# Optimization experiments

Hardware: AMD Instinct MI355X
Metric: run time of the kernel (lower is better)

The kernel has to match this reference:

```python
import jax, jax.numpy as jnp
import numpy as np

T, B, D, H = 256, 2048, 16, 64


def _init_cell(key, in_dim, hidden):
    k1, k2, k3, k4 = jax.random.split(key, 4)
    s = 1.0 / np.sqrt(hidden)
    return (
        jax.random.uniform(k1, (4 * hidden, in_dim), minval=-s, maxval=s),
        jax.random.uniform(k2, (4 * hidden, hidden), minval=-s, maxval=s),
        jax.random.uniform(k3, (4 * hidden,), minval=-s, maxval=s),
        jax.random.uniform(k4, (4 * hidden,), minval=-s, maxval=s),
    )


def setup_inputs() -> dict:
    key = jax.random.key(0)
    kx, k0, k1, k2 = jax.random.split(key, 4)
    x = jax.random.normal(kx, (T, B, D), dtype=jnp.float32)
    W_ih0, W_hh0, b_ih0, b_hh0 = _init_cell(k0, D, H)
    W_ih1, W_hh1, b_ih1, b_hh1 = _init_cell(k1, H, H)
    W_ih2, W_hh2, b_ih2, b_hh2 = _init_cell(k2, H, H)
    return dict(x=x,
                W_ih0=W_ih0, W_hh0=W_hh0, b_ih0=b_ih0, b_hh0=b_hh0,
                W_ih1=W_ih1, W_hh1=W_hh1, b_ih1=b_ih1, b_hh1=b_hh1,
                W_ih2=W_ih2, W_hh2=W_hh2, b_ih2=b_ih2, b_hh2=b_hh2)


def _lstm_cell(x_t, h, c, W_ih, W_hh, b_ih, b_hh):
    # torch.nn.LSTMCell gate order: i, f, g, o
    gates = x_t @ W_ih.T + b_ih + h @ W_hh.T + b_hh  # (B, 4H)
    i, f, g, o = jnp.split(gates, 4, axis=-1)
    c_new = jax.nn.sigmoid(f) * c + jax.nn.sigmoid(i) * jnp.tanh(g)
    h_new = jax.nn.sigmoid(o) * jnp.tanh(c_new)
    return h_new, c_new


def reference(x, W_ih0, W_hh0, b_ih0, b_hh0,
              W_ih1, W_hh1, b_ih1, b_hh1,
              W_ih2, W_hh2, b_ih2, b_hh2):
    Bsz = x.shape[1]
    z = jnp.zeros((Bsz, H), dtype=x.dtype)
    init = (z, z, z, z, z, z)  # h0,h1,h2,c0,c1,c2

    def step(state, x_t):
        h0, h1, h2, c0, c1, c2 = state
        h0, c0 = _lstm_cell(x_t, h0, c0, W_ih0, W_hh0, b_ih0, b_hh0)
        h1, c1 = _lstm_cell(h0, h1, c1, W_ih1, W_hh1, b_ih1, b_hh1)
        h2, c2 = _lstm_cell(h1, h2, c2, W_ih2, W_hh2, b_ih2, b_hh2)
        return (h0, h1, h2, c0, c1, c2), h2

    _, out = jax.lax.scan(step, init, x)  # out: (T, B, H)
    return out
```

## Files before the change

kernel.cpp:

```cpp
#include <hip/hip_runtime.h>
#include <hip/hip_bf16.h>


#define TT 256
#define BB 2048
#define DD 16
#define HH 64

#define SROW 216
#define PANEL (8 * SROW)

typedef __attribute__((ext_vector_type(8))) _Float16 halfx8;
typedef __attribute__((ext_vector_type(8))) unsigned short ushortx8;
typedef __attribute__((ext_vector_type(4))) float floatx4;

#if __has_builtin(__builtin_amdgcn_exp2f)
#define EXP2F(x) __builtin_amdgcn_exp2f(x)
#else
#define EXP2F(x) exp2f(x)
#endif
#if __has_builtin(__builtin_amdgcn_rcpf)
#define RCPF(x) __builtin_amdgcn_rcpf(x)
#else
#define RCPF(x) (1.0f/(x))
#endif

__device__ __forceinline__ float sigm(float x) {
  return RCPF(1.0f + EXP2F(-1.4426950408889634f * x));
}
__device__ __forceinline__ float tanh_f(float x) {
  float xc = fminf(fmaxf(x, -16.0f), 16.0f);
  float t = EXP2F(2.8853900817779268f * xc);
  return 1.0f - 2.0f * RCPF(t + 1.0f);
}
__device__ __forceinline__ void block_sync() {
  asm volatile("s_waitcnt lgkmcnt(0)" ::: "memory");
  __builtin_amdgcn_s_barrier();
}

__global__ void detect_k(const unsigned short* __restrict__ xr, int* __restrict__ flag) {
  int cnt = 0;
  for (int i = threadIdx.x; i < 4096; i += 64) {
    float v = __uint_as_float(((unsigned int)xr[i]) << 16);
    if (!(fabsf(v) < 4.0f)) cnt++;
  }
#pragma unroll
  for (int o = 32; o > 0; o >>= 1) cnt += __shfl_down(cnt, o, 64);
  if (threadIdx.x == 0) flag[0] = (cnt < 100) ? 1 : 0;
}

#define LAYER_MFMA(KSTART, NKT, WA, BS)                                          \
    floatx4 a0 = BS[0], a1 = BS[1];                                              \
    {                                                                            \
      const _Float16* row_ = Pp + rd_row + (KSTART);                             \
      _Pragma("unroll")                                                          \
      for (int kt = 0; kt < (NKT); ++kt) {                                       \
        halfx8 bfr = *(const halfx8*)(row_ + kt * 32 + 8 * g);                   \
        a0 = __builtin_amdgcn_mfma_f32_16x16x32_f16(WA[0][kt], bfr, a0, 0, 0, 0);\
        a1 = __builtin_amdgcn_mfma_f32_16x16x32_f16(WA[1][kt], bfr, a1, 0, 0, 0);\
      }                                                                          \
    }

__launch_bounds__(512, 2)
__global__ void lstm3_k(const void* __restrict__ xg,
                        const void* W0i, const void* W0h, const void* B0i, const void* B0h,
                        const void* W1i, const void* W1h, const void* B1i, const void* B1h,
                        const void* W2i, const void* W2h, const void* B2i, const void* B2h,
                        void* __restrict__ outp, const int* __restrict__ flagp) {
  const int tid = threadIdx.x;
  const int w = tid >> 6;
  const int lane = tid & 63;
  const int c = lane & 15;
  const int g = lane >> 4;
  const int rowbase = blockIdx.x * 8;
  const int isbf = flagp ? flagp[0] : 1;

  __shared__ __align__(16) _Float16 SH[2 * PANEL];

  auto ldf = [&](const void* b, long i) -> float {
    return isbf ? __bfloat162float(((const __hip_bfloat16*)b)[i]) : ((const float*)b)[i];
  };
  auto ld8 = [&](const void* b, long i) -> halfx8 {
    halfx8 r;
    if (isbf) {
      ushortx8 raw = *(const ushortx8*)((const unsigned short*)b + i);
#pragma unroll
      for (int j = 0; j < 8; ++j)
        r[j] = (_Float16)__uint_as_float(((unsigned int)raw[j]) << 16);
    } else {
      const float* s = (const float*)b + i;
#pragma unroll
      for (int j = 0; j < 8; ++j) r[j] = (_Float16)s[j];
    }
    return r;
  };
  auto fragA = [&](const void* Wi, const void* Wh, int Kih, int Mt, int kt) -> halfx8 {
    int ril = Mt * 16 + c;
    int u = ril >> 2, q = ril & 3;
    int orig = q * 64 + u;
    int k0 = kt * 32 + 8 * g;
    if (k0 < Kih) return ld8(Wi, (long)orig * Kih + k0);
    if (k0 < Kih + 64) return ld8(Wh, (long)orig * 64 + (k0 - Kih));
    halfx8 z = {};
    return z;
  };

  halfx8 wA0[2][3], wA1[2][4], wA2[2][4];
  floatx4 bs0[2], bs1[2], bs2[2];
#pragma unroll
  for (int m = 0; m < 2; ++m) {
    const int Mt = 2 * w + m;
#pragma unroll
    for (int kt = 0; kt < 3; ++kt) wA0[m][kt] = fragA(W0i, W0h, 16, Mt, kt);
#pragma unroll
    for (int kt = 0; kt < 4; ++kt) wA1[m][kt] = fragA(W1i, W1h, 64, Mt, kt);
#pragma unroll
    for (int kt = 0; kt < 4; ++kt) wA2[m][kt] = fragA(W2i, W2h, 64, Mt, kt);
    const int ub = 4 * Mt + g;
#pragma unroll
    for (int q = 0; q < 4; ++q) {
      bs0[m][q] = ldf(B0i, 64 * q + ub) + ldf(B0h, 64 * q + ub);
      bs1[m][q] = ldf(B1i, 64 * q + ub) + ldf(B1h, 64 * q + ub);
      bs2[m][q] = ldf(B2i, 64 * q + ub) + ldf(B2h, 64 * q + ub);
    }
  }

  for (int i = tid; i < 2 * PANEL; i += 512) SH[i] = (_Float16)0.0f;
  block_sync();
  if (tid < 16) {
    int r = tid >> 1, hf = tid & 1;
    *(halfx8*)&SH[r * SROW + hf * 8] = ld8(xg, ((long)0 * BB + rowbase + r) * DD + hf * 8);
  }

  const int msel = c >> 3;
  const int r_el = c & 7;
  const int u_el = 8 * w + 4 * msel + g;
  const int rd_row = (c & 7) * SROW;
  const int wr_base = r_el * SROW + u_el;
  float c0s = 0.f, c1s = 0.f, c2s = 0.f;

#pragma unroll 1
  for (int s = 0; s < TT + 2; ++s) {
    const int p = s & 1, np = p ^ 1;
    const _Float16* Pp = SH + p * PANEL;
    _Float16* Pn = SH + np * PANEL;

    halfx8 xreg = {};
    const bool loader = (tid < 16) && (s + 1 < TT);
    if (loader)
      xreg = ld8(xg, ((long)(s + 1) * BB + rowbase + (tid >> 1)) * DD + (tid & 1) * 8);

    block_sync();

    if (s < TT) {
      LAYER_MFMA(0, 3, wA0, bs0)
      floatx4 gv = msel ? a1 : a0;
      float I = sigm(gv[0]), F = sigm(gv[1]), G = tanh_f(gv[2]), O = sigm(gv[3]);
      float cn = F * c0s + I * G; c0s = cn;
      Pn[wr_base + 16] = (_Float16)(O * tanh_f(cn));
    }
    if (s >= 1 && s <= TT) {
      LAYER_MFMA(16, 4, wA1, bs1)
      floatx4 gv = msel ? a1 : a0;
      float I = sigm(gv[0]), F = sigm(gv[1]), G = tanh_f(gv[2]), O = sigm(gv[3]);
      float cn = F * c1s + I * G; c1s = cn;
      Pn[wr_base + 80] = (_Float16)(O * tanh_f(cn));
    }
    if (s >= 2) {
      LAYER_MFMA(80, 4, wA2, bs2)
      floatx4 gv = msel ? a1 : a0;
      float I = sigm(gv[0]), F = sigm(gv[1]), G = tanh_f(gv[2]), O = sigm(gv[3]);
      float cn = F * c2s + I * G; c2s = cn;
      float hn = O * tanh_f(cn);
      Pn[wr_base + 144] = (_Float16)hn;
      size_t oi = ((size_t)(s - 2) * BB + rowbase + r_el) * HH + u_el;
      if (isbf) ((__hip_bfloat16*)outp)[oi] = __float2bfloat16(hn);
      else      ((float*)outp)[oi] = hn;
    }
    if (loader)
      *(halfx8*)&Pn[(tid >> 1) * SROW + (tid & 1) * 8] = xreg;
  }
}

extern "C" void kernel_launch(void* const* d_in, const int* in_sizes, int n_in,
                              void* d_out, int out_size, void* d_ws, size_t ws_size,
                              hipStream_t stream) {
  (void)in_sizes; (void)n_in; (void)out_size;
  int* flag = (ws_size >= sizeof(int)) ? (int*)d_ws : nullptr;
  if (flag) {
    detect_k<<<dim3(1), dim3(64), 0, stream>>>((const unsigned short*)d_in[0], flag);
  }
  lstm3_k<<<dim3(BB / 8), dim3(512), 0, stream>>>(
      d_in[0],
      d_in[1], d_in[2], d_in[3], d_in[4],
      d_in[5], d_in[6], d_in[7], d_in[8],
      d_in[9], d_in[10], d_in[11], d_in[12],
      d_out, flag);
}
```

Baseline: 310.8 us.

## Interleave MFMAs of all three LSTM layers and unroll ping-pong step loop

Reorders the shared panel layout to [h0,h1,h2,x] so each lane loads all seven B fragments once per step. The MFMAs of all three layers are then issued interleaved, so independent accumulator chains hide MFMA latency. Layer-activity branches become predicated stores, the step loop is unrolled by two with constant panel offsets, and the tanh input clamp is removed. The trade-offs are wasted MFMA and transcendental work in the pipeline fill and drain steps, higher register pressure, and possible overflow behaviour in tanh for large inputs.

New measurement: 276.7 us. 1.12x faster.

```diff
diff --git a/kernel.cpp b/kernel.cpp
--- a/kernel.cpp
+++ b/kernel.cpp
@@ -9,6 +9,10 @@
 
 #define SROW 216
 #define PANEL (8 * SROW)
+#define H0O 0
+#define H1O 64
+#define H2O 128
+#define XO  192
 
 typedef __attribute__((ext_vector_type(8))) _Float16 halfx8;
 typedef __attribute__((ext_vector_type(8))) unsigned short ushortx8;
@@ -29,8 +33,7 @@
   return RCPF(1.0f + EXP2F(-1.4426950408889634f * x));
 }
 __device__ __forceinline__ float tanh_f(float x) {
-  float xc = fminf(fmaxf(x, -16.0f), 16.0f);
-  float t = EXP2F(2.8853900817779268f * xc);
+  float t = EXP2F(2.8853900817779268f * x);
   return 1.0f - 2.0f * RCPF(t + 1.0f);
 }
 __device__ __forceinline__ void block_sync() {
@@ -49,17 +52,59 @@
   if (threadIdx.x == 0) flag[0] = (cnt < 100) ? 1 : 0;
 }
 
-#define LAYER_MFMA(KSTART, NKT, WA, BS)                                          \
-    floatx4 a0 = BS[0], a1 = BS[1];                                              \
-    {                                                                            \
-      const _Float16* row_ = Pp + rd_row + (KSTART);                             \
-      _Pragma("unroll")                                                          \
-      for (int kt = 0; kt < (NKT); ++kt) {                                       \
-        halfx8 bfr = *(const halfx8*)(row_ + kt * 32 + 8 * g);                   \
-        a0 = __builtin_amdgcn_mfma_f32_16x16x32_f16(WA[0][kt], bfr, a0, 0, 0, 0);\
-        a1 = __builtin_amdgcn_mfma_f32_16x16x32_f16(WA[1][kt], bfr, a1, 0, 0, 0);\
-      }                                                                          \
-    }
+#define MF(A, B, C) __builtin_amdgcn_mfma_f32_16x16x32_f16(A, B, C, 0, 0, 0)
+
+#define BODY(S_, PPB, PNB)                                                        \
+  {                                                                               \
+    const int s_ = (S_);                                                          \
+    halfx8 xreg = {};                                                             \
+    const bool loader = (tid < 16) && (s_ + 1 < TT);                              \
+    if (loader)                                                                   \
+      xreg = ld8(xg, ((long)(s_ + 1) * BB + rowbase + (tid >> 1)) * DD + (tid & 1) * 8); \
+    block_sync();                                                                 \
+    const _Float16* PpR = SH + (PPB) + rd_off;                                    \
+    _Float16* Pn = SH + (PNB);                                                    \
+    halfx8 r0 = *(const halfx8*)(PpR + 0);                                        \
+    halfx8 r1 = *(const halfx8*)(PpR + 32);                                       \
+    halfx8 r2 = *(const halfx8*)(PpR + 64);                                       \
+    halfx8 r3 = *(const halfx8*)(PpR + 96);                                       \
+    halfx8 r4 = *(const halfx8*)(PpR + 128);                                      \
+    halfx8 r5 = *(const halfx8*)(PpR + 160);                                      \
+    halfx8 r6 = *(const halfx8*)(PpR + 192);                                      \
+    floatx4 a00 = bs0[0], a01 = bs0[1];                                           \
+    floatx4 a10 = bs1[0], a11 = bs1[1];                                           \
+    floatx4 a20 = bs2[0], a21 = bs2[1];                                           \
+    a00 = MF(wA0[0][0], r0, a00); a01 = MF(wA0[1][0], r0, a01);                   \
+    a10 = MF(wA1[0][0], r0, a10); a11 = MF(wA1[1][0], r0, a11);                   \
+    a00 = MF(wA0[0][1], r1, a00); a01 = MF(wA0[1][1], r1, a01);                   \
+    a10 = MF(wA1[0][1], r1, a10); a11 = MF(wA1[1][1], r1, a11);                   \
+    a20 = MF(wA2[0][0], r2, a20); a21 = MF(wA2[1][0], r2, a21);                   \
+    a10 = MF(wA1[0][2], r2, a10); a11 = MF(wA1[1][2], r2, a11);                   \
+    a20 = MF(wA2[0][1], r3, a20); a21 = MF(wA2[1][1], r3, a21);                   \
+    a10 = MF(wA1[0][3], r3, a10); a11 = MF(wA1[1][3], r3, a11);                   \
+    a20 = MF(wA2[0][2], r4, a20); a21 = MF(wA2[1][2], r4, a21);                   \
+    a20 = MF(wA2[0][3], r5, a20); a21 = MF(wA2[1][3], r5, a21);                   \
+    a00 = MF(wA0[0][2], r6, a00); a01 = MF(wA0[1][2], r6, a01);                   \
+    { floatx4 gv = msel ? a01 : a00;                                              \
+      float I = sigm(gv[0]), F = sigm(gv[1]), G = tanh_f(gv[2]), O = sigm(gv[3]); \
+      float cn = F * c0s + I * G;                                                 \
+      float hn = O * tanh_f(cn);                                                  \
+      if (s_ < TT) { c0s = cn; Pn[wr_base + H0O] = (_Float16)hn; } }              \
+    { floatx4 gv = msel ? a11 : a10;                                              \
+      float I = sigm(gv[0]), F = sigm(gv[1]), G = tanh_f(gv[2]), O = sigm(gv[3]); \
+      float cn = F * c1s + I * G;                                                 \
+      float hn = O * tanh_f(cn);                                                  \
+      if (s_ >= 1 && s_ <= TT) { c1s = cn; Pn[wr_base + H1O] = (_Float16)hn; } }  \
+    { floatx4 gv = msel ? a21 : a20;                                              \
+      float I = sigm(gv[0]), F = sigm(gv[1]), G = tanh_f(gv[2]), O = sigm(gv[3]); \
+      float cn = F * c2s + I * G;                                                 \
+      float hn = O * tanh_f(cn);                                                  \
+      if (s_ >= 2) { c2s = cn; Pn[wr_base + H2O] = (_Float16)hn;                  \
+        long oi = (long)(s_ - 2) * ((long)BB * HH) + olane;                       \
+        if (isbf) ((__hip_bfloat16*)outp)[oi] = __float2bfloat16(hn);             \
+        else ((float*)outp)[oi] = hn; } }                                         \
+    if (loader) *(halfx8*)&Pn[(tid >> 1) * SROW + XO + (tid & 1) * 8] = xreg;     \
+  }
 
 __launch_bounds__(512, 2)
 __global__ void lstm3_k(const void* __restrict__ xg,
@@ -75,7 +120,7 @@
   const int rowbase = blockIdx.x * 8;
   const int isbf = flagp ? flagp[0] : 1;
 
-  __shared__ __align__(16) _Float16 SH[2 * PANEL];
+  __shared__ __align__(16) _Float16 SH[2 * PANEL + 32];
 
   auto ldf = [&](const void* b, long i) -> float {
     return isbf ? __bfloat162float(((const __hip_bfloat16*)b)[i]) : ((const float*)b)[i];
@@ -94,91 +139,57 @@
     }
     return r;
   };
-  auto fragA = [&](const void* Wi, const void* Wh, int Kih, int Mt, int kt) -> halfx8 {
-    int ril = Mt * 16 + c;
-    int u = ril >> 2, q = ril & 3;
-    int orig = q * 64 + u;
-    int k0 = kt * 32 + 8 * g;
-    if (k0 < Kih) return ld8(Wi, (long)orig * Kih + k0);
-    if (k0 < Kih + 64) return ld8(Wh, (long)orig * 64 + (k0 - Kih));
-    halfx8 z = {};
-    return z;
-  };
 
   halfx8 wA0[2][3], wA1[2][4], wA2[2][4];
   floatx4 bs0[2], bs1[2], bs2[2];
 #pragma unroll
   for (int m = 0; m < 2; ++m) {
     const int Mt = 2 * w + m;
-#pragma unroll
-    for (int kt = 0; kt < 3; ++kt) wA0[m][kt] = fragA(W0i, W0h, 16, Mt, kt);
-#pragma unroll
-    for (int kt = 0; kt < 4; ++kt) wA1[m][kt] = fragA(W1i, W1h, 64, Mt, kt);
-#pragma unroll
-    for (int kt = 0; kt < 4; ++kt) wA2[m][kt] = fragA(W2i, W2h, 64, Mt, kt);
+    const int ril = Mt * 16 + c;
+    const int u = ril >> 2, q = ril & 3;
+    const long orig = q * 64 + u;
+    halfx8 z = {};
+    wA0[m][0] = ld8(W0h, orig * 64 + 8 * g);
+    wA0[m][1] = ld8(W0h, orig * 64 + 32 + 8 * g);
+    wA0[m][2] = (g == 0) ? ld8(W0i, orig * 16)
+              : (g == 1) ? ld8(W0i, orig * 16 + 8) : z;
+    wA1[m][0] = ld8(W1i, orig * 64 + 8 * g);
+    wA1[m][1] = ld8(W1i, orig * 64 + 32 + 8 * g);
+    wA1[m][2] = ld8(W1h, orig * 64 + 8 * g);
+    wA1[m][3] = ld8(W1h, orig * 64 + 32 + 8 * g);
+    wA2[m][0] = ld8(W2i, orig * 64 + 8 * g);
+    wA2[m][1] = ld8(W2i, orig * 64 + 32 + 8 * g);
+    wA2[m][2] = ld8(W2h, orig * 64 + 8 * g);
+    wA2[m][3] = ld8(W2h, orig * 64 + 32 + 8 * g);
     const int ub = 4 * Mt + g;
 #pragma unroll
-    for (int q = 0; q < 4; ++q) {
-      bs0[m][q] = ldf(B0i, 64 * q + ub) + ldf(B0h, 64 * q + ub);
-      bs1[m][q] = ldf(B1i, 64 * q + ub) + ldf(B1h, 64 * q + ub);
-      bs2[m][q] = ldf(B2i, 64 * q + ub) + ldf(B2h, 64 * q + ub);
+    for (int qq = 0; qq < 4; ++qq) {
+      bs0[m][qq] = ldf(B0i, 64 * qq + ub) + ldf(B0h, 64 * qq + ub);
+      bs1[m][qq] = ldf(B1i, 64 * qq + ub) + ldf(B1h, 64 * qq + ub);
+      bs2[m][qq] = ldf(B2i, 64 * qq + ub) + ldf(B2h, 64 * qq + ub);
     }
   }
 
-  for (int i = tid; i < 2 * PANEL; i += 512) SH[i] = (_Float16)0.0f;
+  for (int i = tid; i < 2 * PANEL + 32; i += 512) SH[i] = (_Float16)0.0f;
   block_sync();
   if (tid < 16) {
-    int r = tid >> 1, hf = tid & 1;
-    *(halfx8*)&SH[r * SROW + hf * 8] = ld8(xg, ((long)0 * BB + rowbase + r) * DD + hf * 8);
+    *(halfx8*)&SH[(tid >> 1) * SROW + XO + (tid & 1) * 8] =
+        ld8(xg, ((long)0 * BB + rowbase + (tid >> 1)) * DD + (tid & 1) * 8);
   }
 
   const int msel = c >> 3;
   const int r_el = c & 7;
   const int u_el = 8 * w + 4 * msel + g;
-  const int rd_row = (c & 7) * SROW;
+  const int rd_off = (c & 7) * SROW + 8 * g;
   const int wr_base = r_el * SROW + u_el;
+  const long olane = ((long)rowbase + r_el) * HH + u_el;
   float c0s = 0.f, c1s = 0.f, c2s = 0.f;
 
 #pragma unroll 1
-  for (int s = 0; s < TT + 2; ++s) {
-    const int p = s & 1, np = p ^ 1;
-    const _Float16* Pp = SH + p * PANEL;
-    _Float16* Pn = SH + np * PANEL;
-
-    halfx8 xreg = {};
-    const bool loader = (tid < 16) && (s + 1 < TT);
-    if (loader)
-      xreg = ld8(xg, ((long)(s + 1) * BB + rowbase + (tid >> 1)) * DD + (tid & 1) * 8);
-
-    block_sync();
-
-    if (s < TT) {
-      LAYER_MFMA(0, 3, wA0, bs0)
-      floatx4 gv = msel ? a1 : a0;
-      float I = sigm(gv[0]), F = sigm(gv[1]), G = tanh_f(gv[2]), O = sigm(gv[3]);
-      float cn = F * c0s + I * G; c0s = cn;
-      Pn[wr_base + 16] = (_Float16)(O * tanh_f(cn));
-    }
-    if (s >= 1 && s <= TT) {
-      LAYER_MFMA(16, 4, wA1, bs1)
-      floatx4 gv = msel ? a1 : a0;
-      float I = sigm(gv[0]), F = sigm(gv[1]), G = tanh_f(gv[2]), O = sigm(gv[3]);
-      float cn = F * c1s + I * G; c1s = cn;
-      Pn[wr_base + 80] = (_Float16)(O * tanh_f(cn));
-    }
-    if (s >= 2) {
-      LAYER_MFMA(80, 4, wA2, bs2)
-      floatx4 gv = msel ? a1 : a0;
-      float I = sigm(gv[0]), F = sigm(gv[1]), G = tanh_f(gv[2]), O = sigm(gv[3]);
-      float cn = F * c2s + I * G; c2s = cn;
-      float hn = O * tanh_f(cn);
-      Pn[wr_base + 144] = (_Float16)hn;
-      size_t oi = ((size_t)(s - 2) * BB + rowbase + r_el) * HH + u_el;
-      if (isbf) ((__hip_bfloat16*)outp)[oi] = __float2bfloat16(hn);
-      else      ((float*)outp)[oi] = hn;
-    }
-    if (loader)
-      *(halfx8*)&Pn[(tid >> 1) * SROW + (tid & 1) * 8] = xreg;
+  for (int s2 = 0; s2 < (TT + 2) / 2; ++s2) {
+    const int s = 2 * s2;
+    BODY(s, 0, PANEL)
+    BODY(s + 1, PANEL, 0)
   }
 }
 
```
